# Kernel optimization log

Hardware: AMD Instinct MI355X
Metric: run time of the kernel (lower is better)

Reference implementation:

```python
import jax, jax.numpy as jnp
import numpy as np

K_STEPS = 2  # number of staged propagation levels encoded in edge_mask


def _propagate(h, src, dst, mask, num_nodes):
    """KPropagate: K staged scatter-add steps over the edge list.

    Step k sums messages along edges with edge_mask == k; later steps
    propagate the freshly aggregated values (rule-node fan-out).
    """
    out = jnp.zeros_like(h)
    cur = h
    for k in range(K_STEPS):
        msg = jnp.where((mask == k)[:, None], cur[src], jnp.zeros((), h.dtype))  # [E, F]
        out = out + jax.ops.segment_sum(msg, dst, num_segments=num_nodes)
        cur = out
    return out


def setup_inputs() -> dict:
    key = jax.random.key(0)
    ks = jax.random.split(key, 8)
    V, R = 50000, 10000
    N = V + R
    E = 160000
    F_IN, F_OUT = 512, 128
    x = jax.random.normal(ks[0], (N, F_IN), dtype=jnp.float32)
    edge_index = jax.random.randint(ks[1], (2, E), 0, N, dtype=jnp.int64)
    edge_mask = jax.random.randint(ks[2], (E,), 0, K_STEPS, dtype=jnp.int64)
    # lin1: in_features -> in_features; lin2: in_features -> out_features
    s1 = 1.0 / np.sqrt(F_IN)
    W1 = jax.random.uniform(ks[3], (F_IN, F_IN), jnp.float32, -s1, s1)
    b1 = jax.random.uniform(ks[4], (F_IN,), jnp.float32, -s1, s1)
    W2 = jax.random.uniform(ks[5], (F_IN, F_OUT), jnp.float32, -s1, s1)
    b2 = jax.random.uniform(ks[6], (F_OUT,), jnp.float32, -s1, s1)
    return {"x": x, "edge_index": edge_index, "edge_mask": edge_mask,
            "vertex_cnt": V, "rule_cnt": R,
            "W1": W1, "b1": b1, "W2": W2, "b2": b2}


def reference(x, edge_index, edge_mask, vertex_cnt, rule_cnt, W1, b1, W2, b2):
    N = x.shape[0]  # == vertex_cnt + rule_cnt
    src, dst = edge_index[0], edge_index[1]
    h = x @ W1 + b1                                   # lin1
    h = jax.nn.relu(_propagate(h, src, dst, edge_mask, N))  # P1 -> relu
    h = h @ W2 + b2                                   # lin2
    h = _propagate(h, src, dst, edge_mask, N)         # P2
    # NOTE: original code computes log_softmax into `out` but returns x (=h).
    return h
```

## Files before the change

kernel.cpp:

```cpp
#include <hip/hip_runtime.h>

typedef __bf16 bf16x8 __attribute__((ext_vector_type(8)));
typedef float  floatx4 __attribute__((ext_vector_type(4)));
typedef unsigned short ushortx8 __attribute__((ext_vector_type(8)));
typedef unsigned short ushortx4 __attribute__((ext_vector_type(4)));
typedef unsigned short ushortx2 __attribute__((ext_vector_type(2)));

__device__ __forceinline__ float bf2f(unsigned short u) {
    return __uint_as_float(((unsigned)u) << 16);
}
__device__ __forceinline__ unsigned short f2bf(float f) {
    unsigned u = __float_as_uint(f);
    return (unsigned short)((u + 0x7FFFu + ((u >> 16) & 1u)) >> 16);
}

__device__ __forceinline__ void gload_lds16(const unsigned short* g, unsigned short* l) {
    __builtin_amdgcn_global_load_lds(
        (const __attribute__((address_space(1))) void*)g,
        (__attribute__((address_space(3))) void*)l, 16, 0, 0);
}

__global__ void cvt_f32_bf16_kernel(const float* __restrict__ in,
                                    unsigned short* __restrict__ out, int n4) {
    int i = blockIdx.x * blockDim.x + threadIdx.x;
    if (i >= n4) return;
    float4 v = ((const float4*)in)[i];
    ushortx4 o;
    o[0] = f2bf(v.x); o[1] = f2bf(v.y); o[2] = f2bf(v.z); o[3] = f2bf(v.w);
    ((ushortx4*)out)[i] = o;
}

__global__ void transpose_cvt_kernel(const float* __restrict__ in,
                                     unsigned short* __restrict__ out,
                                     int K, int N) {
    int idx = blockIdx.x * blockDim.x + threadIdx.x;
    if (idx >= K * N) return;
    int k = idx / N, n = idx - k * N;
    out[n * K + k] = f2bf(in[idx]);
}

__global__ void init_head_kernel(int* __restrict__ head, int n) {
    int i = blockIdx.x * blockDim.x + threadIdx.x;
    if (i < n) head[i] = -1;
}

__global__ void build_list_kernel(const int* __restrict__ ei, const int* __restrict__ em,
                                  int E, int Nn,
                                  int* __restrict__ head, int* __restrict__ nxt) {
    int e = blockIdx.x * blockDim.x + threadIdx.x;
    if (e >= E) return;
    int d = ei[E + e];
    int m = em[e];
    nxt[e] = atomicExch(&head[m * Nn + d], e);
}

#define BM 128
#define BN 128
#define BK 64

__global__ __launch_bounds__(256) void gemm_bt_bias(
    const unsigned short* __restrict__ A,
    const unsigned short* __restrict__ Bt,
    const float* __restrict__ bias,
    unsigned short* __restrict__ C,
    int M, int N, int K)
{
    __shared__ unsigned short Sh[16384];
    unsigned short (*As)[512] = (unsigned short(*)[512])Sh;
    unsigned short (*Bs)[512] = (unsigned short(*)[512])(Sh + 8192);

    const int tid  = threadIdx.x;
    const int lane = tid & 63;
    const int wave = tid >> 6;

    int bx, by;
    if (gridDim.x == 4) {
        int id = blockIdx.y * 4 + blockIdx.x;
        int full = (gridDim.y & ~7) * 4;
        if (id < full) {
            bx = (id >> 3) & 3;
            by = (id >> 5) * 8 + (id & 7);
        } else {
            int t = id - full;
            by = (gridDim.y & ~7) + (t >> 2);
            bx = t & 3;
        }
    } else {
        bx = blockIdx.x; by = blockIdx.y;
    }
    const int bM = by * BM;
    const int bN = bx * BN;
    const int wm = (wave >> 1) * 64;
    const int wn = (wave & 1) * 64;
    const int q    = lane >> 4;
    const int mrow = lane & 15;

    const unsigned short* pA[4];
    const unsigned short* pB[4];
#pragma unroll
    for (int c = 0; c < 4; c++) {
        int gg = wave + 4 * c;
        int g7 = gg & 7, s = gg >> 3;
        int rA = bM + g7 * 16 + mrow; if (rA >= M) rA = M - 1;
        int rB = bN + g7 * 16 + mrow;
        pA[c] = A  + (size_t)rA * K + s * 32 + q * 8;
        pB[c] = Bt + (size_t)rB * K + s * 32 + q * 8;
    }

    floatx4 acc[4][4];
#pragma unroll
    for (int i = 0; i < 4; i++)
#pragma unroll
        for (int j = 0; j < 4; j++) acc[i][j] = (floatx4)(0.0f);

    for (int kt = 0; kt < K; kt += BK) {
#pragma unroll
        for (int c = 0; c < 4; c++) {
            gload_lds16(pA[c] + kt, &As[wave + 4 * c][0]);
            gload_lds16(pB[c] + kt, &Bs[wave + 4 * c][0]);
        }
        __syncthreads();

#pragma unroll
        for (int s = 0; s < 2; s++) {
            bf16x8 af[4], bfv[4];
#pragma unroll
            for (int mi = 0; mi < 4; mi++)
                af[mi] = *(const bf16x8*)&As[s * 8 + (wave >> 1) * 4 + mi][lane * 8];
#pragma unroll
            for (int ni = 0; ni < 4; ni++)
                bfv[ni] = *(const bf16x8*)&Bs[s * 8 + (wave & 1) * 4 + ni][lane * 8];
#pragma unroll
            for (int mi = 0; mi < 4; mi++)
#pragma unroll
                for (int ni = 0; ni < 4; ni++)
                    acc[mi][ni] = __builtin_amdgcn_mfma_f32_16x16x32_bf16(
                        af[mi], bfv[ni], acc[mi][ni], 0, 0, 0);
        }
        __syncthreads();
    }

    unsigned short* lbuf = Sh + wave * 2048;
    float bv[4];
#pragma unroll
    for (int ni = 0; ni < 4; ni++) bv[ni] = bias[bN + wn + ni * 16 + mrow];

#pragma unroll
    for (int p = 0; p < 2; p++) {
#pragma unroll
        for (int mh = 0; mh < 2; mh++) {
            int mi = 2 * p + mh;
#pragma unroll
            for (int ni = 0; ni < 4; ni++)
#pragma unroll
                for (int r = 0; r < 4; r++)
                    lbuf[(mh * 16 + q * 4 + r) * 64 + ni * 16 + mrow] =
                        f2bf(acc[mi][ni][r] + bv[ni]);
        }
#pragma unroll
        for (int i = 0; i < 4; i++) {
            int prow = i * 8 + (lane >> 3);
            int pcol = (lane & 7) * 8;
            int grow = bM + wm + p * 32 + prow;
            if (grow < M)
                *(ushortx8*)(C + (size_t)grow * N + bN + wn + pcol) =
                    *(const ushortx8*)&lbuf[prow * 64 + pcol];
        }
    }
}

template <int VEC> struct VecT;
template <> struct VecT<8> { typedef ushortx8 type; };
template <> struct VecT<2> { typedef ushortx2 type; };

template <int VEC, bool ADD_SELF, bool RELU, bool OUT_F32>
__global__ __launch_bounds__(256) void prop_step_kernel(
    const unsigned short* __restrict__ cur,
    void* __restrict__ outp,
    const int* __restrict__ head,
    const int* __restrict__ nxt,
    const int* __restrict__ esrc,
    int Nn)
{
    typedef typename VecT<VEC>::type VT;
    const int w = blockIdx.x * 4 + (threadIdx.x >> 6);
    if (w >= Nn) return;
    const int lane = threadIdx.x & 63;
    const int F = VEC * 64;
    const size_t off = (size_t)w * F + lane * VEC;

    float acc[VEC];
    if (ADD_SELF) {
        VT v = *(const VT*)(cur + off);
#pragma unroll
        for (int i = 0; i < VEC; i++) acc[i] = bf2f(v[i]);
    } else {
#pragma unroll
        for (int i = 0; i < VEC; i++) acc[i] = 0.0f;
    }

    for (int e = head[w]; e >= 0; e = nxt[e]) {
        int s = esrc[e];
        VT v = *(const VT*)(cur + (size_t)s * F + lane * VEC);
#pragma unroll
        for (int i = 0; i < VEC; i++) acc[i] += bf2f(v[i]);
    }

#pragma unroll
    for (int i = 0; i < VEC; i++)
        if (RELU && acc[i] < 0.0f) acc[i] = 0.0f;

    if (OUT_F32) {
        float* out = (float*)outp;
        float2 o2;
#pragma unroll
        for (int i = 0; i < VEC; i += 2) {
            o2.x = acc[i]; o2.y = acc[i + 1];
            *(float2*)(out + off + i) = o2;
        }
    } else {
        VT o;
#pragma unroll
        for (int i = 0; i < VEC; i++) o[i] = f2bf(acc[i]);
        *(VT*)((unsigned short*)outp + off) = o;
    }
}

extern "C" void kernel_launch(void* const* d_in, const int* in_sizes, int n_in,
                              void* d_out, int out_size, void* d_ws, size_t ws_size,
                              hipStream_t stream)
{
    const float* x  = (const float*)d_in[0];
    const int*   ei = (const int*)d_in[1];
    const int*   em = (const int*)d_in[2];
    const float* W1 = (const float*)d_in[5];
    const float* b1 = (const float*)d_in[6];
    const float* W2 = (const float*)d_in[7];
    const float* b2 = (const float*)d_in[8];

    const int FIN = 512, FOUT = 128;
    const int Nn = in_sizes[0] / FIN;
    const int E  = in_sizes[2];

    char* ws = (char*)d_ws;
    size_t off = 0;
    auto alloc = [&](size_t bytes) -> char* {
        char* p = ws + off;
        off += (bytes + 255) & ~(size_t)255;
        return p;
    };
    unsigned short* W1t = (unsigned short*)alloc((size_t)FIN * FIN * 2);
    unsigned short* W2t = (unsigned short*)alloc((size_t)FIN * FOUT * 2);
    unsigned short* xb  = (unsigned short*)alloc((size_t)Nn * FIN * 2);
    unsigned short* h1  = (unsigned short*)alloc((size_t)Nn * FIN * 2);
    unsigned short* h2  = (unsigned short*)alloc((size_t)Nn * FOUT * 2);
    unsigned short* A2  = (unsigned short*)alloc((size_t)Nn * FOUT * 2);
    int* head = (int*)alloc((size_t)2 * Nn * 4);
    int* nxt  = (int*)alloc((size_t)E * 4);
    unsigned short* A1 = xb;
    (void)ws_size; (void)n_in; (void)out_size;

    cvt_f32_bf16_kernel<<<((Nn * FIN / 4) + 255) / 256, 256, 0, stream>>>(x, xb, Nn * FIN / 4);
    transpose_cvt_kernel<<<(FIN * FIN + 255) / 256, 256, 0, stream>>>(W1, W1t, FIN, FIN);
    transpose_cvt_kernel<<<(FIN * FOUT + 255) / 256, 256, 0, stream>>>(W2, W2t, FIN, FOUT);

    init_head_kernel<<<(2 * Nn + 255) / 256, 256, 0, stream>>>(head, 2 * Nn);
    build_list_kernel<<<(E + 255) / 256, 256, 0, stream>>>(ei, em, E, Nn, head, nxt);

    {
        dim3 grid(FIN / BN, (Nn + BM - 1) / BM);
        gemm_bt_bias<<<grid, 256, 0, stream>>>(xb, W1t, b1, h1, Nn, FIN, FIN);
    }

    {
        int grid = (Nn + 3) / 4;
        prop_step_kernel<8, false, false, false><<<grid, 256, 0, stream>>>(h1, A1, head,      nxt, ei, Nn);
        prop_step_kernel<8, true,  true,  false><<<grid, 256, 0, stream>>>(A1, h1, head + Nn, nxt, ei, Nn);
    }

    {
        dim3 grid(FOUT / BN, (Nn + BM - 1) / BM);
        gemm_bt_bias<<<grid, 256, 0, stream>>>(h1, W2t, b2, h2, Nn, FOUT, FIN);
    }

    {
        int grid = (Nn + 3) / 4;
        prop_step_kernel<2, false, false, false><<<grid, 256, 0, stream>>>(h2, A2, head,      nxt, ei, Nn);
        prop_step_kernel<2, true,  false, true ><<<grid, 256, 0, stream>>>(A2, d_out, head + Nn, nxt, ei, Nn);
    }
}
```

Baseline: 398.1 us.

## Fuse fp32-to-bf16 conversion into GEMM A loads with double-buffered B staging

Result: slower. 451.5 us (+13.4%).

```diff
diff --git a/kernel.cpp b/kernel.cpp
--- a/kernel.cpp
+++ b/kernel.cpp
@@ -3,7 +3,6 @@
 typedef __bf16 bf16x8 __attribute__((ext_vector_type(8)));
 typedef float  floatx4 __attribute__((ext_vector_type(4)));
 typedef unsigned short ushortx8 __attribute__((ext_vector_type(8)));
-typedef unsigned short ushortx4 __attribute__((ext_vector_type(4)));
 typedef unsigned short ushortx2 __attribute__((ext_vector_type(2)));
 
 __device__ __forceinline__ float bf2f(unsigned short u) {
@@ -18,16 +17,6 @@
     __builtin_amdgcn_global_load_lds(
         (const __attribute__((address_space(1))) void*)g,
         (__attribute__((address_space(3))) void*)l, 16, 0, 0);
-}
-
-__global__ void cvt_f32_bf16_kernel(const float* __restrict__ in,
-                                    unsigned short* __restrict__ out, int n4) {
-    int i = blockIdx.x * blockDim.x + threadIdx.x;
-    if (i >= n4) return;
-    float4 v = ((const float4*)in)[i];
-    ushortx4 o;
-    o[0] = f2bf(v.x); o[1] = f2bf(v.y); o[2] = f2bf(v.z); o[3] = f2bf(v.w);
-    ((ushortx4*)out)[i] = o;
 }
 
 __global__ void transpose_cvt_kernel(const float* __restrict__ in,
@@ -54,96 +43,122 @@
     nxt[e] = atomicExch(&head[m * Nn + d], e);
 }
 
-#define BM 128
-#define BN 128
-#define BK 64
-
-__global__ __launch_bounds__(256) void gemm_bt_bias(
-    const unsigned short* __restrict__ A,
+template<int NI, bool AF32>
+__global__ __launch_bounds__(256, 3) void gemm_direct(
+    const void* __restrict__ Ap,
     const unsigned short* __restrict__ Bt,
     const float* __restrict__ bias,
     unsigned short* __restrict__ C,
     int M, int N, int K)
 {
-    __shared__ unsigned short Sh[16384];
-    unsigned short (*As)[512] = (unsigned short(*)[512])Sh;
-    unsigned short (*Bs)[512] = (unsigned short(*)[512])(Sh + 8192);
+    constexpr int GB = 2 * NI;
+    constexpr int NGROUP = 4 * NI;
+    __shared__ unsigned short Sh[2 * NGROUP * 512];
 
     const int tid  = threadIdx.x;
     const int lane = tid & 63;
     const int wave = tid >> 6;
 
     int bx, by;
-    if (gridDim.x == 4) {
-        int id = blockIdx.y * 4 + blockIdx.x;
-        int full = (gridDim.y & ~7) * 4;
+    {
+        int gx = gridDim.x;
+        int id = blockIdx.y * gx + blockIdx.x;
+        int rows8 = gridDim.y & ~7;
+        int full = rows8 * gx;
         if (id < full) {
-            bx = (id >> 3) & 3;
-            by = (id >> 5) * 8 + (id & 7);
+            int per = gx * 8;
+            int t = id / per, r = id - t * per;
+            bx = r >> 3; by = t * 8 + (r & 7);
         } else {
             int t = id - full;
-            by = (gridDim.y & ~7) + (t >> 2);
-            bx = t & 3;
-        }
-    } else {
-        bx = blockIdx.x; by = blockIdx.y;
-    }
-    const int bM = by * BM;
-    const int bN = bx * BN;
+            by = rows8 + t / gx; bx = t - (t / gx) * gx;
+        }
+    }
+    const int bM = by * 128;
+    const int bN = bx * (NI * 32);
     const int wm = (wave >> 1) * 64;
-    const int wn = (wave & 1) * 64;
+    const int wn = (wave & 1) * (NI * 16);
     const int q    = lane >> 4;
     const int mrow = lane & 15;
 
-    const unsigned short* pA[4];
-    const unsigned short* pB[4];
-#pragma unroll
-    for (int c = 0; c < 4; c++) {
+    const char* pa[4];
+    constexpr int esz = AF32 ? 4 : 2;
+#pragma unroll
+    for (int mi = 0; mi < 4; mi++) {
+        int r = bM + wm + mi * 16 + mrow; if (r >= M) r = M - 1;
+        pa[mi] = (const char*)Ap + ((size_t)r * K + q * 8) * esz;
+    }
+    const unsigned short* pb[NI];
+#pragma unroll
+    for (int c = 0; c < NI; c++) {
         int gg = wave + 4 * c;
-        int g7 = gg & 7, s = gg >> 3;
-        int rA = bM + g7 * 16 + mrow; if (rA >= M) rA = M - 1;
-        int rB = bN + g7 * 16 + mrow;
-        pA[c] = A  + (size_t)rA * K + s * 32 + q * 8;
-        pB[c] = Bt + (size_t)rB * K + s * 32 + q * 8;
-    }
-
-    floatx4 acc[4][4];
+        int g = gg & (GB - 1), s = gg / GB;
+        int rB = bN + g * 16 + mrow;
+        pb[c] = Bt + (size_t)rB * K + s * 32 + q * 8;
+    }
+
+    floatx4 acc[4][NI];
 #pragma unroll
     for (int i = 0; i < 4; i++)
 #pragma unroll
-        for (int j = 0; j < 4; j++) acc[i][j] = (floatx4)(0.0f);
-
-    for (int kt = 0; kt < K; kt += BK) {
-#pragma unroll
-        for (int c = 0; c < 4; c++) {
-            gload_lds16(pA[c] + kt, &As[wave + 4 * c][0]);
-            gload_lds16(pB[c] + kt, &Bs[wave + 4 * c][0]);
-        }
+        for (int j = 0; j < NI; j++) acc[i][j] = (floatx4)(0.0f);
+
+    auto stage = [&](int k) {
+        unsigned short* base = Sh + (size_t)(k & 1) * NGROUP * 512;
+        int kt = k * 64;
+#pragma unroll
+        for (int c = 0; c < NI; c++)
+            gload_lds16(pb[c] + kt, base + (wave + 4 * c) * 512);
+    };
+
+    const int KI = K >> 6;
+    stage(0);
+    for (int k = 0; k < KI; k++) {
         __syncthreads();
-
+        if (k + 1 < KI) stage(k + 1);
+        const int kt = k * 64;
+
+        bf16x8 af[2][4];
+#pragma unroll
+        for (int s = 0; s < 2; s++)
+#pragma unroll
+            for (int mi = 0; mi < 4; mi++) {
+                if (AF32) {
+                    const float* p = (const float*)pa[mi] + kt + s * 32;
+                    float4 u0 = *(const float4*)p;
+                    float4 u1 = *(const float4*)(p + 4);
+                    bf16x8 t;
+                    t[0] = (__bf16)u0.x; t[1] = (__bf16)u0.y;
+                    t[2] = (__bf16)u0.z; t[3] = (__bf16)u0.w;
+                    t[4] = (__bf16)u1.x; t[5] = (__bf16)u1.y;
+                    t[6] = (__bf16)u1.z; t[7] = (__bf16)u1.w;
+                    af[s][mi] = t;
+                } else {
+                    af[s][mi] = *(const bf16x8*)((const unsigned short*)pa[mi] + (kt + s * 32) * 1);
+                }
+            }
+
+        const unsigned short* base = Sh + (size_t)(k & 1) * NGROUP * 512;
 #pragma unroll
         for (int s = 0; s < 2; s++) {
-            bf16x8 af[4], bfv[4];
+            bf16x8 bfv[NI];
+#pragma unroll
+            for (int ni = 0; ni < NI; ni++)
+                bfv[ni] = *(const bf16x8*)(base + (s * GB + (wave & 1) * NI + ni) * 512 + lane * 8);
 #pragma unroll
             for (int mi = 0; mi < 4; mi++)
-                af[mi] = *(const bf16x8*)&As[s * 8 + (wave >> 1) * 4 + mi][lane * 8];
-#pragma unroll
-            for (int ni = 0; ni < 4; ni++)
-                bfv[ni] = *(const bf16x8*)&Bs[s * 8 + (wave & 1) * 4 + ni][lane * 8];
-#pragma unroll
-            for (int mi = 0; mi < 4; mi++)
-#pragma unroll
-                for (int ni = 0; ni < 4; ni++)
+#pragma unroll
+                for (int ni = 0; ni < NI; ni++)
                     acc[mi][ni] = __builtin_amdgcn_mfma_f32_16x16x32_bf16(
-                        af[mi], bfv[ni], acc[mi][ni], 0, 0, 0);
-        }
-        __syncthreads();
-    }
-
-    unsigned short* lbuf = Sh + wave * 2048;
-    float bv[4];
-#pragma unroll
-    for (int ni = 0; ni < 4; ni++) bv[ni] = bias[bN + wn + ni * 16 + mrow];
+                        af[s][mi], bfv[ni], acc[mi][ni], 0, 0, 0);
+        }
+    }
+
+    constexpr int W = NI * 16;
+    unsigned short* lbuf = Sh + wave * 32 * W;
+    float bv[NI];
+#pragma unroll
+    for (int ni = 0; ni < NI; ni++) bv[ni] = bias[bN + wn + ni * 16 + mrow];
 
 #pragma unroll
     for (int p = 0; p < 2; p++) {
@@ -151,20 +166,22 @@
         for (int mh = 0; mh < 2; mh++) {
             int mi = 2 * p + mh;
 #pragma unroll
-            for (int ni = 0; ni < 4; ni++)
+            for (int ni = 0; ni < NI; ni++)
 #pragma unroll
                 for (int r = 0; r < 4; r++)
-                    lbuf[(mh * 16 + q * 4 + r) * 64 + ni * 16 + mrow] =
+                    lbuf[(mh * 16 + q * 4 + r) * W + ni * 16 + mrow] =
                         f2bf(acc[mi][ni][r] + bv[ni]);
         }
-#pragma unroll
-        for (int i = 0; i < 4; i++) {
-            int prow = i * 8 + (lane >> 3);
-            int pcol = (lane & 7) * 8;
+        constexpr int LPR = W / 8;
+        constexpr int RPI = 64 / LPR;
+#pragma unroll
+        for (int i = 0; i < 32 / RPI; i++) {
+            int prow = i * RPI + lane / LPR;
+            int pcol = (lane % LPR) * 8;
             int grow = bM + wm + p * 32 + prow;
             if (grow < M)
                 *(ushortx8*)(C + (size_t)grow * N + bN + wn + pcol) =
-                    *(const ushortx8*)&lbuf[prow * 64 + pcol];
+                    *(const ushortx8*)&lbuf[prow * W + pcol];
         }
     }
 }
@@ -251,26 +268,24 @@
     };
     unsigned short* W1t = (unsigned short*)alloc((size_t)FIN * FIN * 2);
     unsigned short* W2t = (unsigned short*)alloc((size_t)FIN * FOUT * 2);
-    unsigned short* xb  = (unsigned short*)alloc((size_t)Nn * FIN * 2);
     unsigned short* h1  = (unsigned short*)alloc((size_t)Nn * FIN * 2);
+    unsigned short* A1  = (unsigned short*)alloc((size_t)Nn * FIN * 2);
     unsigned short* h2  = (unsigned short*)alloc((size_t)Nn * FOUT * 2);
     unsigned short* A2  = (unsigned short*)alloc((size_t)Nn * FOUT * 2);
     int* head = (int*)alloc((size_t)2 * Nn * 4);
     int* nxt  = (int*)alloc((size_t)E * 4);
-    unsigned short* A1 = xb;
     (void)ws_size; (void)n_in; (void)out_size;
 
-    cvt_f32_bf16_kernel<<<((Nn * FIN / 4) + 255) / 256, 256, 0, stream>>>(x, xb, Nn * FIN / 4);
     transpose_cvt_kernel<<<(FIN * FIN + 255) / 256, 256, 0, stream>>>(W1, W1t, FIN, FIN);
     transpose_cvt_kernel<<<(FIN * FOUT + 255) / 256, 256, 0, stream>>>(W2, W2t, FIN, FOUT);
 
     init_head_kernel<<<(2 * Nn + 255) / 256, 256, 0, stream>>>(head, 2 * Nn);
     build_list_kernel<<<(E + 255) / 256, 256, 0, stream>>>(ei, em, E, Nn, head, nxt);
 
-    {
-        dim3 grid(FIN / BN, (Nn + BM - 1) / BM);
-        gemm_bt_bias<<<grid, 256, 0, stream>>>(xb, W1t, b1, h1, Nn, FIN, FIN);
-    }
+    const int gy = (Nn + 127) / 128;
+
+    gemm_direct<4, true><<<dim3(FIN / 128, gy), 256, 0, stream>>>(
+        (const void*)x, W1t, b1, h1, Nn, FIN, FIN);
 
     {
         int grid = (Nn + 3) / 4;
@@ -278,10 +293,8 @@
         prop_step_kernel<8, true,  true,  false><<<grid, 256, 0, stream>>>(A1, h1, head + Nn, nxt, ei, Nn);
     }
 
-    {
-        dim3 grid(FOUT / BN, (Nn + BM - 1) / BM);
-        gemm_bt_bias<<<grid, 256, 0, stream>>>(h1, W2t, b2, h2, Nn, FOUT, FIN);
-    }
+    gemm_direct<2, false><<<dim3(FOUT / 64, gy), 256, 0, stream>>>(
+        (const void*)h1, W2t, b2, h2, Nn, FOUT, FIN);
 
     {
         int grid = (Nn + 3) / 4;
```
